# Performance work log

Hardware: AMD Instinct MI355X
Metric: run time of the kernel (lower is better)

The kernel has to match this reference:

```python
import jax, jax.numpy as jnp
import numpy as np

MUL = 512
IR_DIMS = (1, 3, 5)          # 0e, 1e, 2e -> 2l+1
PW = MUL ** -0.5             # path_weight = (mul_in * n_paths_to_out)^-0.5, n_paths=1 each


def setup_inputs() -> dict:
    key = jax.random.key(0)
    k_x, k0, k1, k2 = jax.random.split(key, 4)
    B = 4096
    D = MUL * sum(IR_DIMS)  # 4608
    return {
        "x": jax.random.normal(k_x, (B, D), dtype=jnp.float32),
        "w0": jax.random.normal(k0, (MUL, MUL), dtype=jnp.float32),
        "w1": jax.random.normal(k1, (MUL, MUL), dtype=jnp.float32),
        "w2": jax.random.normal(k2, (MUL, MUL), dtype=jnp.float32),
        "b0": jnp.zeros((MUL,), dtype=jnp.float32),  # bias only on scalar 0e irrep
    }


def reference(x, w0, w1, w2, b0):
    B = x.shape[0]
    # split x into per-irrep blocks (B, mul, 2l+1), as Irreps.as_list does
    offs = np.cumsum([0] + [MUL * d for d in IR_DIMS])
    blocks = [x[:, offs[i]:offs[i + 1]].reshape(B, MUL, IR_DIMS[i]) for i in range(3)]
    outs = []
    for blk, w, d in zip(blocks, (w0, w1, w2), IR_DIMS):
        # path_weight * einsum('uw,bui->bwi'), then flatten to mul_ir_out.dim
        o = PW * jnp.einsum('uw,bui->bwi', w, blk)
        outs.append(o.reshape(B, MUL * d))
    # bias instruction: path_weight 1.0, only on the scalar (0e) output irrep
    outs[0] = outs[0] + b0[None, :]
    return jnp.concatenate(outs, axis=-1)
```

## Files before the change

### kernel.cpp

```cpp
#include <hip/hip_runtime.h>


#define BATCH 4096
#define DTOT 4608
#define NMUL 512

typedef __attribute__((ext_vector_type(8))) short short8;
typedef __attribute__((ext_vector_type(8))) unsigned short ushort8;
typedef __attribute__((ext_vector_type(4))) float float4v;

#define XPL_BYTES (9ull * BATCH * NMUL * 2)

__device__ __forceinline__ unsigned short f2bf(float f) {
    unsigned int u = __builtin_bit_cast(unsigned int, f);
    return (unsigned short)((u + 0x7fffu + ((u >> 16) & 1u)) >> 16);
}
__device__ __forceinline__ void gld16(const unsigned short* g, unsigned short* l) {
    __builtin_amdgcn_global_load_lds(
        (const __attribute__((address_space(1))) unsigned int*)(const void*)g,
        (__attribute__((address_space(3))) unsigned int*)(void*)l, 16, 0, 0);
}
__device__ __forceinline__ void colmap(int col, int& c, int& u) {
    if (col < 512)       { c = 0; u = col; }
    else if (col < 2048) { int t = col - 512;  c = 1 + t % 3; u = t / 3; }
    else                 { int t = col - 2048; c = 4 + t % 5; u = t / 5; }
}

__global__ __launch_bounds__(256) void deint_x(const float* __restrict__ x,
                                               unsigned short* __restrict__ Xp) {
    const int row = blockIdx.x;
    __shared__ unsigned short buf[DTOT];
    const int tid = threadIdx.x;
    const float4v* src = (const float4v*)(x + (size_t)row * DTOT);
    for (int p = tid; p < DTOT / 4; p += 256) {
        float4v v = src[p];
#pragma unroll
        for (int j = 0; j < 4; ++j) {
            int c, u; colmap(p * 4 + j, c, u);
            buf[c * NMUL + u] = f2bf(v[j]);
        }
    }
    __syncthreads();
    for (int q = tid; q < DTOT / 8; q += 256) {
        const int c = q >> 6, u8 = q & 63;
        *(ushort8*)(Xp + ((size_t)(c * BATCH + row) * NMUL) + u8 * 8) =
            *(const ushort8*)&buf[c * NMUL + u8 * 8];
    }
}

__global__ __launch_bounds__(256) void conv_w(const float* __restrict__ w0,
                                              const float* __restrict__ w1,
                                              const float* __restrict__ w2,
                                              unsigned short* __restrict__ Wt) {
    const int b = blockIdx.x;
    const int ch = b >> 6, t = b & 63;
    const int tk = (t >> 3) * 64, tn = (t & 7) * 64;
    const float* W = (ch == 0) ? w0 : (ch == 1) ? w1 : w2;
    __shared__ unsigned short tile[64][72];
    const int tid = threadIdx.x;
    const int r0 = tid >> 4, c4 = (tid & 15) * 4;
#pragma unroll
    for (int rr = 0; rr < 4; ++rr) {
        const int row = r0 + rr * 16;
        float4v v = *(const float4v*)(W + (size_t)(tk + row) * NMUL + tn + c4);
#pragma unroll
        for (int j = 0; j < 4; ++j) tile[c4 + j][row] = f2bf(v[j]);
    }
    __syncthreads();
    for (int q = tid; q < 512; q += 256) {
        const int nn = q >> 3, k8 = q & 7;
        *(ushort8*)(Wt + ((size_t)(ch * NMUL + tn + nn) * NMUL) + tk + k8 * 8) =
            *(const ushort8*)&tile[nn][k8 * 8];
    }
}

__global__ __launch_bounds__(256) void gemm_d1(const unsigned short* __restrict__ Xp,
                                               const unsigned short* __restrict__ Wt,
                                               const float* __restrict__ b0,
                                               float* __restrict__ out) {
    const int n0 = blockIdx.x * 128;
    const int m0 = blockIdx.y * 128;
    __shared__ unsigned short As[128 * 32];
    __shared__ unsigned short Bs[128 * 32];

    const int tid = threadIdx.x;
    const int lane = tid & 63;
    const int w = tid >> 6;
    const int lr = lane & 15;
    const int lq = lane >> 4;
    const int wm = (w >> 1) * 64;
    const int wn = (w & 1) * 64;

    const unsigned short* Ag = Xp + (size_t)(m0 + w * 32 + (lane >> 2)) * NMUL + (lane & 3) * 8;
    const unsigned short* Bg = Wt + (size_t)(n0 + w * 32 + (lane >> 2)) * NMUL + (lane & 3) * 8;
    unsigned short* Al = As + w * 1024;
    unsigned short* Bl = Bs + w * 1024;

    float4v acc[4][4];
#pragma unroll
    for (int a = 0; a < 4; ++a)
#pragma unroll
        for (int b = 0; b < 4; ++b) acc[a][b] = (float4v)0.f;

    for (int kt = 0; kt < 16; ++kt) {
        const int ko = kt * 32;
        gld16(Ag + ko, Al);
        gld16(Ag + ko + 16 * NMUL, Al + 512);
        gld16(Bg + ko, Bl);
        gld16(Bg + ko + 16 * NMUL, Bl + 512);
        __syncthreads();
        short8 af[4], bf[4];
#pragma unroll
        for (int mi = 0; mi < 4; ++mi)
            af[mi] = *(const short8*)(As + (wm + mi * 16 + lr) * 32 + lq * 8);
#pragma unroll
        for (int ni = 0; ni < 4; ++ni)
            bf[ni] = *(const short8*)(Bs + (wn + ni * 16 + lr) * 32 + lq * 8);
#pragma unroll
        for (int mi = 0; mi < 4; ++mi)
#pragma unroll
            for (int ni = 0; ni < 4; ++ni)
                acc[mi][ni] = __builtin_amdgcn_mfma_f32_16x16x32_bf16(
                    af[mi], bf[ni], acc[mi][ni], 0, 0, 0);
        __syncthreads();
    }

    const float PW = 0.044194173824159216f;
#pragma unroll
    for (int ni = 0; ni < 4; ++ni) {
        const int col = n0 + wn + ni * 16 + lr;
        const float bias = b0[col];
#pragma unroll
        for (int mi = 0; mi < 4; ++mi)
#pragma unroll
            for (int r = 0; r < 4; ++r)
                out[(size_t)(m0 + wm + mi * 16 + lq * 4 + r) * DTOT + col] =
                    acc[mi][ni][r] * PW + bias;
    }
}

template <int D, int PBASE, int XOFF, int WCH>
__global__ __launch_bounds__(D * 64) void gemm_d35(
    const unsigned short* __restrict__ Xp,
    const unsigned short* __restrict__ Wt,
    float* __restrict__ out)
{
    __shared__ unsigned short As[D * 2048];
    __shared__ unsigned short Bs[2048];
    float* Cs = (float*)As;

    const int tid = threadIdx.x;
    const int lane = tid & 63;
    const int w = tid >> 6;
    const int lr = lane & 15;
    const int lq = lane >> 4;

    const int n0 = blockIdx.x * 64;
    const int m0 = blockIdx.y * 64;

    const unsigned short* Ag =
        Xp + ((size_t)(PBASE + w) * BATCH + m0 + (lane >> 2)) * NMUL + (lane & 3) * 8;
    const unsigned short* Bg =
        Wt + ((size_t)WCH * NMUL + n0 + (lane >> 2)) * NMUL + (lane & 3) * 8;
    unsigned short* Al = As + w * 2048;

    float4v acc[4][4];
#pragma unroll
    for (int a = 0; a < 4; ++a)
#pragma unroll
        for (int b = 0; b < 4; ++b) acc[a][b] = (float4v)0.f;

    for (int kt = 0; kt < 16; ++kt) {
        const int ko = kt * 32;
#pragma unroll
        for (int p = 0; p < 4; ++p)
            gld16(Ag + (size_t)p * 16 * NMUL + ko, Al + p * 512);
        for (int p = w; p < 4; p += D)
            gld16(Bg + (size_t)p * 16 * NMUL + ko, Bs + p * 512);
        __syncthreads();
        short8 af[4], bf[4];
#pragma unroll
        for (int mi = 0; mi < 4; ++mi)
            af[mi] = *(const short8*)(Al + (mi * 16 + lr) * 32 + lq * 8);
#pragma unroll
        for (int ni = 0; ni < 4; ++ni)
            bf[ni] = *(const short8*)(Bs + (ni * 16 + lr) * 32 + lq * 8);
#pragma unroll
        for (int mi = 0; mi < 4; ++mi)
#pragma unroll
            for (int ni = 0; ni < 4; ++ni)
                acc[mi][ni] = __builtin_amdgcn_mfma_f32_16x16x32_bf16(
                    af[mi], bf[ni], acc[mi][ni], 0, 0, 0);
        __syncthreads();
    }

    const float PW = 0.044194173824159216f;
#pragma unroll
    for (int mc = 0; mc < 4; ++mc) {
#pragma unroll
        for (int ni = 0; ni < 4; ++ni)
#pragma unroll
            for (int r = 0; r < 4; ++r)
                Cs[(lq * 4 + r) * (64 * D) + (ni * 16 + lr) * D + w] =
                    acc[mc][ni][r] * PW;
        __syncthreads();
        constexpr int F4 = 16 * 16 * D;
        for (int f = tid; f < F4; f += D * 64) {
            const int row = f / (16 * D);
            const int c4  = f % (16 * D);
            *(float4v*)(out + (size_t)(m0 + mc * 16 + row) * DTOT + XOFF + n0 * D + c4 * 4) =
                *(const float4v*)(Cs + f * 4);
        }
        __syncthreads();
    }
}

extern "C" void kernel_launch(void* const* d_in, const int* in_sizes, int n_in,
                              void* d_out, int out_size, void* d_ws, size_t ws_size,
                              hipStream_t stream) {
    const float* x  = (const float*)d_in[0];
    const float* w0 = (const float*)d_in[1];
    const float* w1 = (const float*)d_in[2];
    const float* w2 = (const float*)d_in[3];
    const float* b0 = (const float*)d_in[4];
    float* out = (float*)d_out;

    unsigned short* Xp = (unsigned short*)d_ws;
    unsigned short* Wt = (unsigned short*)((char*)d_ws + XPL_BYTES);

    deint_x<<<dim3(BATCH), dim3(256), 0, stream>>>(x, Xp);
    conv_w<<<dim3(192), dim3(256), 0, stream>>>(w0, w1, w2, Wt);
    gemm_d35<5, 4, 2048, 2><<<dim3(8, 64), dim3(320), 0, stream>>>(Xp, Wt, out);
    gemm_d35<3, 1, 512, 1><<<dim3(8, 64), dim3(192), 0, stream>>>(Xp, Wt, out);
    gemm_d1<<<dim3(4, 32), dim3(256), 0, stream>>>(Xp, Wt, b0, out);
}
```

Before: 204.1 us.

## Merge prep kernels and the three GEMM launches into two launches

Combines the x deinterleave and weight conversion into one prep kernel, and runs the d5, d3 and d1 GEMMs from a single 320-thread kernel that picks its work by block index. The aim is to cut launch overhead and the tail gaps between dependent kernels, so blocks from different GEMMs can run on the GPU at the same time. In exchange, the d3 and d1 blocks leave idle waves, since 320 threads are launched but only 192 or 256 do work. The shared allocation is sized for the largest case, which can lower occupancy for the smaller bodies.

```diff
diff --git a/kernel.cpp b/kernel.cpp
--- a/kernel.cpp
+++ b/kernel.cpp
@@ -26,63 +26,140 @@
     else                 { int t = col - 2048; c = 4 + t % 5; u = t / 5; }
 }
 
-__global__ __launch_bounds__(256) void deint_x(const float* __restrict__ x,
-                                               unsigned short* __restrict__ Xp) {
-    const int row = blockIdx.x;
-    __shared__ unsigned short buf[DTOT];
+__global__ __launch_bounds__(256) void prep(const float* __restrict__ x,
+                                            const float* __restrict__ w0,
+                                            const float* __restrict__ w1,
+                                            const float* __restrict__ w2,
+                                            unsigned short* __restrict__ Xp,
+                                            unsigned short* __restrict__ Wt) {
+    __shared__ unsigned short buf[4608];
     const int tid = threadIdx.x;
-    const float4v* src = (const float4v*)(x + (size_t)row * DTOT);
-    for (int p = tid; p < DTOT / 4; p += 256) {
-        float4v v = src[p];
-#pragma unroll
-        for (int j = 0; j < 4; ++j) {
-            int c, u; colmap(p * 4 + j, c, u);
-            buf[c * NMUL + u] = f2bf(v[j]);
-        }
-    }
-    __syncthreads();
-    for (int q = tid; q < DTOT / 8; q += 256) {
-        const int c = q >> 6, u8 = q & 63;
-        *(ushort8*)(Xp + ((size_t)(c * BATCH + row) * NMUL) + u8 * 8) =
-            *(const ushort8*)&buf[c * NMUL + u8 * 8];
-    }
-}
-
-__global__ __launch_bounds__(256) void conv_w(const float* __restrict__ w0,
-                                              const float* __restrict__ w1,
-                                              const float* __restrict__ w2,
-                                              unsigned short* __restrict__ Wt) {
     const int b = blockIdx.x;
-    const int ch = b >> 6, t = b & 63;
-    const int tk = (t >> 3) * 64, tn = (t & 7) * 64;
-    const float* W = (ch == 0) ? w0 : (ch == 1) ? w1 : w2;
-    __shared__ unsigned short tile[64][72];
+    if (b < BATCH) {
+        const int row = b;
+        const float4v* src = (const float4v*)(x + (size_t)row * DTOT);
+        for (int p = tid; p < DTOT / 4; p += 256) {
+            float4v v = src[p];
+#pragma unroll
+            for (int j = 0; j < 4; ++j) {
+                int c, u; colmap(p * 4 + j, c, u);
+                buf[c * NMUL + u] = f2bf(v[j]);
+            }
+        }
+        __syncthreads();
+        for (int q = tid; q < DTOT / 8; q += 256) {
+            const int c = q >> 6, u8 = q & 63;
+            *(ushort8*)(Xp + ((size_t)(c * BATCH + row) * NMUL) + u8 * 8) =
+                *(const ushort8*)&buf[c * NMUL + u8 * 8];
+        }
+    } else {
+        const int t = b - BATCH;
+        const int ch = t >> 6, tt = t & 63;
+        const int tk = (tt >> 3) * 64, tn = (tt & 7) * 64;
+        const float* W = (ch == 0) ? w0 : (ch == 1) ? w1 : w2;
+        const int r0 = tid >> 4, c4 = (tid & 15) * 4;
+#pragma unroll
+        for (int rr = 0; rr < 4; ++rr) {
+            const int row = r0 + rr * 16;
+            float4v v = *(const float4v*)(W + (size_t)(tk + row) * NMUL + tn + c4);
+#pragma unroll
+            for (int j = 0; j < 4; ++j) buf[(c4 + j) * 72 + row] = f2bf(v[j]);
+        }
+        __syncthreads();
+        for (int q = tid; q < 512; q += 256) {
+            const int nn = q >> 3, k8 = q & 7;
+            *(ushort8*)(Wt + ((size_t)(ch * NMUL + tn + nn) * NMUL) + tk + k8 * 8) =
+                *(const ushort8*)&buf[nn * 72 + k8 * 8];
+        }
+    }
+}
+
+template <int D, int PBASE, int XOFF, int WCH>
+__device__ __forceinline__ void body_d35(int rel,
+                                         const unsigned short* __restrict__ Xp,
+                                         const unsigned short* __restrict__ Wt,
+                                         float* __restrict__ out,
+                                         unsigned short* As, unsigned short* Bs) {
+    float* Cs = (float*)As;
+
     const int tid = threadIdx.x;
-    const int r0 = tid >> 4, c4 = (tid & 15) * 4;
-#pragma unroll
-    for (int rr = 0; rr < 4; ++rr) {
-        const int row = r0 + rr * 16;
-        float4v v = *(const float4v*)(W + (size_t)(tk + row) * NMUL + tn + c4);
-#pragma unroll
-        for (int j = 0; j < 4; ++j) tile[c4 + j][row] = f2bf(v[j]);
-    }
-    __syncthreads();
-    for (int q = tid; q < 512; q += 256) {
-        const int nn = q >> 3, k8 = q & 7;
-        *(ushort8*)(Wt + ((size_t)(ch * NMUL + tn + nn) * NMUL) + tk + k8 * 8) =
-            *(const ushort8*)&tile[nn][k8 * 8];
-    }
-}
-
-__global__ __launch_bounds__(256) void gemm_d1(const unsigned short* __restrict__ Xp,
-                                               const unsigned short* __restrict__ Wt,
-                                               const float* __restrict__ b0,
-                                               float* __restrict__ out) {
-    const int n0 = blockIdx.x * 128;
-    const int m0 = blockIdx.y * 128;
-    __shared__ unsigned short As[128 * 32];
-    __shared__ unsigned short Bs[128 * 32];
-
+    const int lane = tid & 63;
+    const int w = tid >> 6;
+    const int lr = lane & 15;
+    const int lq = lane >> 4;
+
+    const int n0 = (rel & 7) * 64;
+    const int m0 = (rel >> 3) * 64;
+
+    const unsigned short* Ag =
+        Xp + ((size_t)(PBASE + w) * BATCH + m0 + (lane >> 2)) * NMUL + (lane & 3) * 8;
+    const unsigned short* Bg =
+        Wt + ((size_t)WCH * NMUL + n0 + (lane >> 2)) * NMUL + (lane & 3) * 8;
+    unsigned short* Al = As + w * 2048;
+
+    float4v acc[4][4];
+#pragma unroll
+    for (int a = 0; a < 4; ++a)
+#pragma unroll
+        for (int b = 0; b < 4; ++b) acc[a][b] = (float4v)0.f;
+
+    for (int kt = 0; kt < 16; ++kt) {
+        const int ko = kt * 32;
+        if (w < D) {
+#pragma unroll
+            for (int p = 0; p < 4; ++p)
+                gld16(Ag + (size_t)p * 16 * NMUL + ko, Al + p * 512);
+            for (int p = w; p < 4; p += D)
+                gld16(Bg + (size_t)p * 16 * NMUL + ko, Bs + p * 512);
+        }
+        __syncthreads();
+        if (w < D) {
+            short8 af[4], bf[4];
+#pragma unroll
+            for (int mi = 0; mi < 4; ++mi)
+                af[mi] = *(const short8*)(Al + (mi * 16 + lr) * 32 + lq * 8);
+#pragma unroll
+            for (int ni = 0; ni < 4; ++ni)
+                bf[ni] = *(const short8*)(Bs + (ni * 16 + lr) * 32 + lq * 8);
+#pragma unroll
+            for (int mi = 0; mi < 4; ++mi)
+#pragma unroll
+                for (int ni = 0; ni < 4; ++ni)
+                    acc[mi][ni] = __builtin_amdgcn_mfma_f32_16x16x32_bf16(
+                        af[mi], bf[ni], acc[mi][ni], 0, 0, 0);
+        }
+        __syncthreads();
+    }
+
+    const float PW = 0.044194173824159216f;
+#pragma unroll
+    for (int mc = 0; mc < 4; ++mc) {
+        if (w < D) {
+#pragma unroll
+            for (int ni = 0; ni < 4; ++ni)
+#pragma unroll
+                for (int r = 0; r < 4; ++r)
+                    Cs[(lq * 4 + r) * (64 * D) + (ni * 16 + lr) * D + w] =
+                        acc[mc][ni][r] * PW;
+        }
+        __syncthreads();
+        constexpr int F4 = 16 * 16 * D;
+        for (int f = tid; f < F4; f += 320) {
+            const int row = f / (16 * D);
+            const int c4  = f % (16 * D);
+            *(float4v*)(out + (size_t)(m0 + mc * 16 + row) * DTOT + XOFF + n0 * D + c4 * 4) =
+                *(const float4v*)(Cs + f * 4);
+        }
+        __syncthreads();
+    }
+}
+
+__device__ __forceinline__ void body_d1(int rel,
+                                        const unsigned short* __restrict__ Xp,
+                                        const unsigned short* __restrict__ Wt,
+                                        const float* __restrict__ b0,
+                                        float* __restrict__ out,
+                                        unsigned short* As, unsigned short* Bs) {
     const int tid = threadIdx.x;
     const int lane = tid & 63;
     const int w = tid >> 6;
@@ -91,6 +168,9 @@
     const int wm = (w >> 1) * 64;
     const int wn = (w & 1) * 64;
 
+    const int n0 = (rel & 3) * 128;
+    const int m0 = (rel >> 2) * 128;
+
     const unsigned short* Ag = Xp + (size_t)(m0 + w * 32 + (lane >> 2)) * NMUL + (lane & 3) * 8;
     const unsigned short* Bg = Wt + (size_t)(n0 + w * 32 + (lane >> 2)) * NMUL + (lane & 3) * 8;
     unsigned short* Al = As + w * 1024;
@@ -104,115 +184,58 @@
 
     for (int kt = 0; kt < 16; ++kt) {
         const int ko = kt * 32;
-        gld16(Ag + ko, Al);
-        gld16(Ag + ko + 16 * NMUL, Al + 512);
-        gld16(Bg + ko, Bl);
-        gld16(Bg + ko + 16 * NMUL, Bl + 512);
-        __syncthreads();
-        short8 af[4], bf[4];
-#pragma unroll
-        for (int mi = 0; mi < 4; ++mi)
-            af[mi] = *(const short8*)(As + (wm + mi * 16 + lr) * 32 + lq * 8);
-#pragma unroll
-        for (int ni = 0; ni < 4; ++ni)
-            bf[ni] = *(const short8*)(Bs + (wn + ni * 16 + lr) * 32 + lq * 8);
-#pragma unroll
-        for (int mi = 0; mi < 4; ++mi)
+        if (w < 4) {
+            gld16(Ag + ko, Al);
+            gld16(Ag + ko + 16 * NMUL, Al + 512);
+            gld16(Bg + ko, Bl);
+            gld16(Bg + ko + 16 * NMUL, Bl + 512);
+        }
+        __syncthreads();
+        if (w < 4) {
+            short8 af[4], bf[4];
+#pragma unroll
+            for (int mi = 0; mi < 4; ++mi)
+                af[mi] = *(const short8*)(As + (wm + mi * 16 + lr) * 32 + lq * 8);
 #pragma unroll
             for (int ni = 0; ni < 4; ++ni)
-                acc[mi][ni] = __builtin_amdgcn_mfma_f32_16x16x32_bf16(
-                    af[mi], bf[ni], acc[mi][ni], 0, 0, 0);
-        __syncthreads();
-    }
-
-    const float PW = 0.044194173824159216f;
-#pragma unroll
-    for (int ni = 0; ni < 4; ++ni) {
-        const int col = n0 + wn + ni * 16 + lr;
-        const float bias = b0[col];
-#pragma unroll
-        for (int mi = 0; mi < 4; ++mi)
-#pragma unroll
-            for (int r = 0; r < 4; ++r)
-                out[(size_t)(m0 + wm + mi * 16 + lq * 4 + r) * DTOT + col] =
-                    acc[mi][ni][r] * PW + bias;
-    }
-}
-
-template <int D, int PBASE, int XOFF, int WCH>
-__global__ __launch_bounds__(D * 64) void gemm_d35(
-    const unsigned short* __restrict__ Xp,
-    const unsigned short* __restrict__ Wt,
-    float* __restrict__ out)
-{
-    __shared__ unsigned short As[D * 2048];
-    __shared__ unsigned short Bs[2048];
-    float* Cs = (float*)As;
-
-    const int tid = threadIdx.x;
-    const int lane = tid & 63;
-    const int w = tid >> 6;
-    const int lr = lane & 15;
-    const int lq = lane >> 4;
-
-    const int n0 = blockIdx.x * 64;
-    const int m0 = blockIdx.y * 64;
-
-    const unsigned short* Ag =
-        Xp + ((size_t)(PBASE + w) * BATCH + m0 + (lane >> 2)) * NMUL + (lane & 3) * 8;
-    const unsigned short* Bg =
-        Wt + ((size_t)WCH * NMUL + n0 + (lane >> 2)) * NMUL + (lane & 3) * 8;
-    unsigned short* Al = As + w * 2048;
-
-    float4v acc[4][4];
-#pragma unroll
-    for (int a = 0; a < 4; ++a)
-#pragma unroll
-        for (int b = 0; b < 4; ++b) acc[a][b] = (float4v)0.f;
-
-    for (int kt = 0; kt < 16; ++kt) {
-        const int ko = kt * 32;
-#pragma unroll
-        for (int p = 0; p < 4; ++p)
-            gld16(Ag + (size_t)p * 16 * NMUL + ko, Al + p * 512);
-        for (int p = w; p < 4; p += D)
-            gld16(Bg + (size_t)p * 16 * NMUL + ko, Bs + p * 512);
-        __syncthreads();
-        short8 af[4], bf[4];
-#pragma unroll
-        for (int mi = 0; mi < 4; ++mi)
-            af[mi] = *(const short8*)(Al + (mi * 16 + lr) * 32 + lq * 8);
-#pragma unroll
-        for (int ni = 0; ni < 4; ++ni)
-            bf[ni] = *(const short8*)(Bs + (ni * 16 + lr) * 32 + lq * 8);
-#pragma unroll
-        for (int mi = 0; mi < 4; ++mi)
-#pragma unroll
-            for (int ni = 0; ni < 4; ++ni)
-                acc[mi][ni] = __builtin_amdgcn_mfma_f32_16x16x32_bf16(
-                    af[mi], bf[ni], acc[mi][ni], 0, 0, 0);
-        __syncthreads();
-    }
-
-    const float PW = 0.044194173824159216f;
-#pragma unroll
-    for (int mc = 0; mc < 4; ++mc) {
-#pragma unroll
-        for (int ni = 0; ni < 4; ++ni)
-#pragma unroll
-            for (int r = 0; r < 4; ++r)
-                Cs[(lq * 4 + r) * (64 * D) + (ni * 16 + lr) * D + w] =
-                    acc[mc][ni][r] * PW;
-        __syncthreads();
-        constexpr int F4 = 16 * 16 * D;
-        for (int f = tid; f < F4; f += D * 64) {
-            const int row = f / (16 * D);
-            const int c4  = f % (16 * D);
-            *(float4v*)(out + (size_t)(m0 + mc * 16 + row) * DTOT + XOFF + n0 * D + c4 * 4) =
-                *(const float4v*)(Cs + f * 4);
-        }
-        __syncthreads();
-    }
+                bf[ni] = *(const short8*)(Bs + (wn + ni * 16 + lr) * 32 + lq * 8);
+#pragma unroll
+            for (int mi = 0; mi < 4; ++mi)
+#pragma unroll
+                for (int ni = 0; ni < 4; ++ni)
+                    acc[mi][ni] = __builtin_amdgcn_mfma_f32_16x16x32_bf16(
+                        af[mi], bf[ni], acc[mi][ni], 0, 0, 0);
+        }
+        __syncthreads();
+    }
+
+    if (w < 4) {
+        const float PW = 0.044194173824159216f;
+#pragma unroll
+        for (int ni = 0; ni < 4; ++ni) {
+            const int col = n0 + wn + ni * 16 + lr;
+            const float bias = b0[col];
+#pragma unroll
+            for (int mi = 0; mi < 4; ++mi)
+#pragma unroll
+                for (int r = 0; r < 4; ++r)
+                    out[(size_t)(m0 + wm + mi * 16 + lq * 4 + r) * DTOT + col] =
+                        acc[mi][ni][r] * PW + bias;
+        }
+    }
+}
+
+__global__ __launch_bounds__(320) void gemm_all(const unsigned short* __restrict__ Xp,
+                                                const unsigned short* __restrict__ Wt,
+                                                const float* __restrict__ b0,
+                                                float* __restrict__ out) {
+    __shared__ __align__(16) unsigned short As[10240];
+    __shared__ __align__(16) unsigned short Bs[4096];
+
+    const int b = blockIdx.x;
+    if (b < 512)       body_d35<5, 4, 2048, 2>(b, Xp, Wt, out, As, Bs);
+    else if (b < 1024) body_d35<3, 1, 512, 1>(b - 512, Xp, Wt, out, As, Bs);
+    else               body_d1(b - 1024, Xp, Wt, b0, out, As, Bs);
 }
 
 extern "C" void kernel_launch(void* const* d_in, const int* in_sizes, int n_in,
@@ -228,9 +251,6 @@
     unsigned short* Xp = (unsigned short*)d_ws;
     unsigned short* Wt = (unsigned short*)((char*)d_ws + XPL_BYTES);
 
-    deint_x<<<dim3(BATCH), dim3(256), 0, stream>>>(x, Xp);
-    conv_w<<<dim3(192), dim3(256), 0, stream>>>(w0, w1, w2, Wt);
-    gemm_d35<5, 4, 2048, 2><<<dim3(8, 64), dim3(320), 0, stream>>>(Xp, Wt, out);
-    gemm_d35<3, 1, 512, 1><<<dim3(8, 64), dim3(192), 0, stream>>>(Xp, Wt, out);
-    gemm_d1<<<dim3(4, 32), dim3(256), 0, stream>>>(Xp, Wt, b0, out);
-}
+    prep<<<dim3(BATCH + 192), dim3(256), 0, stream>>>(x, w0, w1, w2, Xp, Wt);
+    gemm_all<<<dim3(1152), dim3(320), 0, stream>>>(Xp, Wt, b0, out);
+}
```

After: 192.8 us. 5.5% less time.
